# Kernel tuning notes

Measured on AMD Instinct MI355X. Metric: run time of the kernel, lower is better.

## Reference

```python
import jax, jax.numpy as jnp
import numpy as np
from jax import lax

B, C, H, W = 8, 128, 64, 64
L = H * W  # 4096, multiple of 64 so BiMamba2's pad-to-chunk is a no-op
DM, DI, DS, DC, NH, HD = 32, 64, 64, 4, 1, 64  # d_model, d_inner, d_state, d_conv, nheads, headdim


def setup_inputs() -> dict:
    key = jax.random.key(0)
    ks = jax.random.split(key, 12)
    def r(i, shape, s):
        return jax.random.normal(ks[i], shape, jnp.float32) * s
    return {
        "x": jax.random.normal(ks[0], (B, C, H, W), jnp.float32),
        "lin1_w": r(1, (C, C), 0.05), "lin1_b": jnp.zeros((C,), jnp.float32),
        "dw_w": r(2, (C, 1, 3, 3), 0.1), "dw_b": jnp.zeros((C,), jnp.float32),
        "fc_in_w": r(3, (C, DM), 0.05),
        "mam_in_w": r(4, (2, DM, 2 * DI + 2 * DS + NH), 0.05),
        "mam_conv_w": r(5, (2, DI + 2 * DS, DC), 0.1),
        "mam_conv_b": jnp.zeros((2, DI + 2 * DS), jnp.float32),
        "mam_dt_bias": r(6, (2, NH), 0.1),
        "mam_A_log": jnp.zeros((2, NH), jnp.float32),
        "mam_D": jnp.ones((2, NH), jnp.float32),
        "mam_norm_w": jnp.ones((2, DI), jnp.float32),
        "mam_out_w": r(7, (2, DI, DM), 0.05),
        "fc_out_w": r(8, (DM, C), 0.05),
        "bn_g": jnp.ones((C,), jnp.float32), "bn_b": jnp.zeros((C,), jnp.float32),
        "conv4_w": r(9, (C, C), 0.05), "conv4_b": jnp.zeros((C,), jnp.float32),
    }


def _causal_dwconv1d(x, w, b):
    # x: (B, L, Ch); w: (Ch, DC) depthwise causal kernel (torch Conv1d groups=Ch, pad=DC-1, trimmed)
    xc = jnp.transpose(x, (0, 2, 1))
    xc = jnp.pad(xc, ((0, 0), (0, 0), (DC - 1, 0)))
    o = lax.conv_general_dilated(xc, w[:, None, :], (1,), "VALID",
                                 feature_group_count=w.shape[0],
                                 dimension_numbers=("NCH", "OIH", "NCH"))
    return jnp.transpose(o + b[None, :, None], (0, 2, 1))


def _mamba2(u, W_in, conv_w, conv_b, dt_bias, A_log, D, norm_w, W_out):
    # u: (B, L, DM). Minimal Mamba2 block: in_proj -> causal dwconv/silu -> selective scan -> gated RMSNorm -> out_proj
    b, l, _ = u.shape
    zxbcdt = u @ W_in                         # (b, l, 2*DI + 2*DS + NH)
    z = zxbcdt[..., :DI]
    xBC = zxbcdt[..., DI:DI + DI + 2 * DS]
    dt = zxbcdt[..., -NH:]
    xBC = jax.nn.silu(_causal_dwconv1d(xBC, conv_w, conv_b))
    xs = xBC[..., :DI]
    Bm = xBC[..., DI:DI + DS]                 # (b, l, DS)
    Cm = xBC[..., DI + DS:]                   # (b, l, DS)
    dt = jax.nn.softplus(dt + dt_bias)        # (b, l, NH)
    dA = jnp.exp(dt * (-jnp.exp(A_log)))      # (b, l, NH)
    xh = xs.reshape(b, l, NH, HD)
    dtx = dt[..., None] * xh                  # (b, l, NH, HD)

    def step(h, inp):
        dA_t, dtx_t, B_t, C_t = inp
        h = dA_t[:, :, None, None] * h + dtx_t[..., None] * B_t[:, None, None, :]
        y = jnp.einsum("bhpn,bn->bhp", h, C_t)
        return h, y

    h0 = jnp.zeros((b, NH, HD, DS), u.dtype)
    _, ys = lax.scan(step, h0, (jnp.moveaxis(dA, 1, 0), jnp.moveaxis(dtx, 1, 0),
                                jnp.moveaxis(Bm, 1, 0), jnp.moveaxis(Cm, 1, 0)))
    y = jnp.moveaxis(ys, 0, 1) + D[None, None, :, None] * xh   # (b, l, NH, HD)
    y = y.reshape(b, l, DI)
    y = y * jax.nn.silu(z)                    # gated RMSNorm
    y = y * lax.rsqrt(jnp.mean(y * y, -1, keepdims=True) + 1e-5) * norm_w
    return y @ W_out                          # (b, l, DM)


def _forward(x, lin1_w, lin1_b, dw_w, dw_b, fc_in_w, mam_in_w, mam_conv_w, mam_conv_b,
             mam_dt_bias, mam_A_log, mam_D, mam_norm_w, mam_out_w, fc_out_w,
             bn_g, bn_b, conv4_w, conv4_b):
    b, c, h, w = x.shape
    o = jnp.einsum("bihw,io->bohw", x, lin1_w) + lin1_b[None, :, None, None]
    o = lax.conv_general_dilated(o, dw_w, (1, 1), "SAME", feature_group_count=c,
                                 dimension_numbers=("NCHW", "OIHW", "NCHW")) + dw_b[None, :, None, None]
    o = jax.nn.silu(o)
    # BiMamba2_2D: flatten HxW -> sequence, fc_in, forward + reversed Mamba2, fc_out
    s = jnp.einsum("bcl,cd->bld", o.reshape(b, c, h * w), fc_in_w)
    y1 = _mamba2(s, mam_in_w[0], mam_conv_w[0], mam_conv_b[0], mam_dt_bias[0],
                 mam_A_log[0], mam_D[0], mam_norm_w[0], mam_out_w[0])
    y2 = jnp.flip(_mamba2(jnp.flip(s, 1), mam_in_w[1], mam_conv_w[1], mam_conv_b[1],
                          mam_dt_bias[1], mam_A_log[1], mam_D[1], mam_norm_w[1], mam_out_w[1]), 1)
    o = jnp.transpose((y1 + y2) @ fc_out_w, (0, 2, 1)).reshape(b, c, h, w)
    # BatchNorm2d (training-mode batch statistics)
    mu = jnp.mean(o, (0, 2, 3), keepdims=True)
    var = jnp.mean((o - mu) ** 2, (0, 2, 3), keepdims=True)
    o = (o - mu) * lax.rsqrt(var + 1e-5) * bn_g[None, :, None, None] + bn_b[None, :, None, None]
    g = jax.nn.sigmoid(jnp.einsum("bihw,io->bohw", o, conv4_w) + conv4_b[None, :, None, None])
    return g * x + x


def reference(x, lin1_w, lin1_b, dw_w, dw_b, fc_in_w, mam_in_w, mam_conv_w, mam_conv_b,
              mam_dt_bias, mam_A_log, mam_D, mam_norm_w, mam_out_w, fc_out_w,
              bn_g, bn_b, conv4_w, conv4_b):
    return _forward(x, lin1_w, lin1_b, dw_w, dw_b, fc_in_w, mam_in_w, mam_conv_w, mam_conv_b,
                    mam_dt_bias, mam_A_log, mam_D, mam_norm_w, mam_out_w, fc_out_w,
                    bn_g, bn_b, conv4_w, conv4_b)
```

## Files before the change

kernel.cpp:

```cpp
#include <hip/hip_runtime.h>
#include <math.h>

constexpr int Bn = 8, Cn = 128, Ln = 4096;

constexpr size_t OFF_O1   = 0;
constexpr size_t OFF_O2   = 4194304;
constexpr size_t OFF_S    = 8388608;
constexpr size_t OFF_Z    = 9437184;
constexpr size_t OFF_WT   = 11534336;
constexpr size_t OFF_XBCA = 13631488;
constexpr size_t OFF_DTS  = 26214400;
constexpr size_t OFF_CUM  = 26279936;
constexpr size_t OFF_T    = 26345472;
constexpr size_t OFF_SPREV= 30539776;
constexpr size_t OFF_S2A  = 34734080;
constexpr size_t OFF_S2B  = 35782656;
constexpr size_t OFF_BN   = 36831232;
constexpr size_t OFF_O3   = 0;

constexpr long XSTRIDE_H = 6291456;
constexpr long TSTRIDE = 2097152;

typedef __attribute__((ext_vector_type(8))) short short8;
typedef __attribute__((ext_vector_type(4))) float f32x4;
typedef __attribute__((ext_vector_type(4))) unsigned short us4;
typedef __attribute__((ext_vector_type(8))) unsigned short us8;

__device__ __forceinline__ float siluf(float v) { return v / (1.0f + expf(-v)); }

__device__ __forceinline__ unsigned short tobf(float f) {
  unsigned int u = __float_as_uint(f);
  u += 0x7FFFu + ((u >> 16) & 1u);
  return (unsigned short)(u >> 16);
}

__device__ __forceinline__ float frombf(unsigned short u) {
  return __uint_as_float(((unsigned int)u) << 16);
}

__device__ __forceinline__ unsigned int pk2(float a, float b) {
  return (unsigned int)tobf(a) | ((unsigned int)tobf(b) << 16);
}

__device__ __forceinline__ short8 ldfrag(const unsigned short* p) {
  union { unsigned int u[4]; short8 s; } cv;
  cv.u[0] = *(const unsigned int*)(p);
  cv.u[1] = *(const unsigned int*)(p + 2);
  cv.u[2] = *(const unsigned int*)(p + 4);
  cv.u[3] = *(const unsigned int*)(p + 6);
  return cv.s;
}

__global__ __launch_bounds__(256) void k_lin1(const float* __restrict__ x,
                                              const float* __restrict__ w,
                                              const float* __restrict__ bias,
                                              unsigned short* __restrict__ o1) {
  __shared__ unsigned short wT[64][140];
  __shared__ unsigned short xT[64][140];
  int b = blockIdx.y, l0 = blockIdx.x * 64, cb = blockIdx.z * 64;
  int tid = threadIdx.x, lane = tid & 63, mt = tid >> 6;
  int q = lane >> 4, i = lane & 15;
  int c4 = (tid & 15) * 4, k0 = (tid >> 4) * 2;
#pragma unroll
  for (int s = 0; s < 4; ++s) {
    int k = k0 + s * 32;
    float4 w0 = *(const float4*)&w[k * 128 + cb + c4];
    float4 w1 = *(const float4*)&w[(k + 1) * 128 + cb + c4];
    *(unsigned int*)&wT[c4 + 0][k] = pk2(w0.x, w1.x);
    *(unsigned int*)&wT[c4 + 1][k] = pk2(w0.y, w1.y);
    *(unsigned int*)&wT[c4 + 2][k] = pk2(w0.z, w1.z);
    *(unsigned int*)&wT[c4 + 3][k] = pk2(w0.w, w1.w);
    float4 x0 = *(const float4*)&x[((long)b * 128 + k) * 4096 + l0 + c4];
    float4 x1 = *(const float4*)&x[((long)b * 128 + k + 1) * 4096 + l0 + c4];
    *(unsigned int*)&xT[c4 + 0][k] = pk2(x0.x, x1.x);
    *(unsigned int*)&xT[c4 + 1][k] = pk2(x0.y, x1.y);
    *(unsigned int*)&xT[c4 + 2][k] = pk2(x0.z, x1.z);
    *(unsigned int*)&xT[c4 + 3][k] = pk2(x0.w, x1.w);
  }
  __syncthreads();
  short8 af[4];
#pragma unroll
  for (int kk = 0; kk < 4; ++kk)
    af[kk] = ldfrag(&wT[mt * 16 + i][q * 8 + 32 * kk]);
  float bv[4];
#pragma unroll
  for (int r2 = 0; r2 < 4; ++r2) bv[r2] = bias[cb + 16 * mt + q * 4 + r2];
#pragma unroll
  for (int nt = 0; nt < 4; ++nt) {
    f32x4 d = {0.f, 0.f, 0.f, 0.f};
#pragma unroll
    for (int kk = 0; kk < 4; ++kk) {
      short8 bfr = ldfrag(&xT[nt * 16 + i][q * 8 + 32 * kk]);
      d = __builtin_amdgcn_mfma_f32_16x16x32_bf16(af[kk], bfr, d, 0, 0, 0);
    }
#pragma unroll
    for (int r2 = 0; r2 < 4; ++r2) {
      int c = 16 * mt + q * 4 + r2;
      o1[((long)b * 128 + cb + c) * 4096 + l0 + nt * 16 + i] = tobf(d[r2] + bv[r2]);
    }
  }
}

__global__ void k_dw(const unsigned short* __restrict__ o1,
                     const float* __restrict__ wgt,
                     const float* __restrict__ bias, unsigned short* __restrict__ o2) {
  __shared__ float p[4096];
  int bc = blockIdx.x, c = bc & 127, tid = threadIdx.x;
  const unsigned short* src = o1 + (long)bc * 4096;
#pragma unroll
  for (int s4 = 0; s4 < 2; ++s4) {
    int off = s4 * 2048 + tid * 8;
    us8 v = *(const us8*)&src[off];
#pragma unroll
    for (int j = 0; j < 8; ++j) p[off + j] = frombf(v[j]);
  }
  float wr[9];
#pragma unroll
  for (int j = 0; j < 9; ++j) wr[j] = wgt[c * 9 + j];
  float bv = bias[c];
  __syncthreads();
  int wg = tid & 15, hs = tid >> 4;
  int w0 = wg * 4, h0 = hs * 4;
  float in[6][6];
#pragma unroll
  for (int ri = 0; ri < 6; ++ri) {
    int h = h0 - 1 + ri;
    if (h < 0 || h > 63) {
#pragma unroll
      for (int ci = 0; ci < 6; ++ci) in[ri][ci] = 0.f;
    } else {
      float4 cc = *(float4*)&p[h * 64 + w0];
      in[ri][1] = cc.x; in[ri][2] = cc.y; in[ri][3] = cc.z; in[ri][4] = cc.w;
      in[ri][0] = (w0 > 0) ? p[h * 64 + w0 - 1] : 0.f;
      in[ri][5] = (w0 < 60) ? p[h * 64 + w0 + 4] : 0.f;
    }
  }
#pragma unroll
  for (int r = 0; r < 4; ++r) {
    us4 oc;
#pragma unroll
    for (int q = 0; q < 4; ++q) {
      float acc = bv;
#pragma unroll
      for (int dh = 0; dh < 3; ++dh)
#pragma unroll
        for (int dq = 0; dq < 3; ++dq)
          acc += in[r + dh][q + dq] * wr[dh * 3 + dq];
      oc[q] = tobf(siluf(acc));
    }
    *(us4*)&o2[(long)bc * 4096 + (h0 + r) * 64 + w0] = oc;
  }
}

__global__ void k_fcin(const unsigned short* __restrict__ o2, const float* __restrict__ w,
                       unsigned short* __restrict__ sb,
                       const float* __restrict__ Win, unsigned short* __restrict__ WT) {
  __shared__ float xt[128][64];
  __shared__ float wt[128][32];
  int b = blockIdx.y, l0 = blockIdx.x * 64;
  int tid = threadIdx.x;
  int f4 = (tid & 15) * 4, r0 = tid >> 4;
#pragma unroll
  for (int st = 0; st < 8; ++st) {
    int r = r0 + st * 16;
    us4 v = *(const us4*)&o2[((long)b * 128 + r) * 4096 + l0 + f4];
#pragma unroll
    for (int j = 0; j < 4; ++j) xt[r][f4 + j] = frombf(v[j]);
  }
  int f4w = (tid & 7) * 4, rw = tid >> 3;
#pragma unroll
  for (int st = 0; st < 4; ++st) {
    int r = rw + st * 32;
    *(float4*)&wt[r][f4w] = *(const float4*)&w[r * 32 + f4w];
  }
  __syncthreads();
  int tx = tid & 15, ty = tid >> 4;
  int c0 = tx * 4, d0 = ty * 2;
  float acc[2][4] = {};
  for (int k = 0; k < 128; ++k) {
    float4 xv = *(float4*)&xt[k][c0];
    float2 wv = *(float2*)&wt[k][d0];
    float xa[4] = {xv.x, xv.y, xv.z, xv.w};
#pragma unroll
    for (int q = 0; q < 4; ++q) {
      acc[0][q] += wv.x * xa[q];
      acc[1][q] += wv.y * xa[q];
    }
  }
#pragma unroll
  for (int q = 0; q < 4; ++q) {
    long ob = ((long)b * 4096 + l0 + c0 + q) * 32 + d0;
    *(unsigned int*)&sb[ob] = pk2(acc[0][q], acc[1][q]);
  }
  if (blockIdx.y == 0 && blockIdx.x < 2) {
    int dir = blockIdx.x;
    for (int idx = tid; idx < 272 * 32; idx += 256) {
      int n = idx >> 5, kk = idx & 31;
      float v = (n < 257) ? Win[dir * 32 * 257 + kk * 257 + n] : 0.f;
      WT[dir * 8704 + idx] = tobf(v);
    }
  }
}

__global__ __launch_bounds__(256) void k_inprojconv(
    const unsigned short* __restrict__ sb, const unsigned short* __restrict__ WT,
    const float* __restrict__ conv_w, const float* __restrict__ conv_b,
    const float* __restrict__ dt_bias, const float* __restrict__ A_log,
    unsigned short* __restrict__ zT, unsigned short* __restrict__ xbca,
    float* __restrict__ dts, float* __restrict__ cum, float* __restrict__ Tg) {
  __shared__ unsigned short xbcT[192][82];
  __shared__ float fXf[64][68];
  __shared__ float dtL[64];
  __shared__ float dtsS[64], cumSS[64], fL[64];
  int dir = blockIdx.z, b = blockIdx.y, l0 = blockIdx.x * 64;
  int tid = threadIdx.x, lane = tid & 63, mt = tid >> 6;
  int q = lane >> 4, i = lane & 15;
  long rowbase = (long)b * 4096 + l0;
  const unsigned short* W = WT + (long)dir * 8704;
  const short8 zfrag = {0, 0, 0, 0, 0, 0, 0, 0};

  if (mt == 0) {
    short8 afr[4];
#pragma unroll
    for (int rt = 0; rt < 4; ++rt) {
      int l = l0 + 16 * rt + i;
      int lsrc = dir ? (4095 - l) : l;
      afr[rt] = *(const short8*)&sb[((long)b * 4096 + lsrc) * 32 + q * 8];
    }
#pragma unroll
    for (int ct = 0; ct < 4; ++ct) {
      int n = 16 * ct + i;
      short8 bfr = *(const short8*)&W[n * 32 + q * 8];
      unsigned short* zrow = zT + (((long)dir * 64 + n) * 8 + b) * 4096 + l0 + q * 4;
#pragma unroll
      for (int rt = 0; rt < 4; ++rt) {
        f32x4 d = {0.f, 0.f, 0.f, 0.f};
        d = __builtin_amdgcn_mfma_f32_16x16x32_bf16(afr[rt], bfr, d, 0, 0, 0);
        us4 pk;
        pk[0] = tobf(d[0]); pk[1] = tobf(d[1]);
        pk[2] = tobf(d[2]); pk[3] = tobf(d[3]);
        *(us4*)&zrow[16 * rt] = pk;
      }
    }
    {
      short8 bfr = *(const short8*)&W[(256 + i) * 32 + q * 8];
#pragma unroll
      for (int rt = 0; rt < 4; ++rt) {
        f32x4 d = {0.f, 0.f, 0.f, 0.f};
        d = __builtin_amdgcn_mfma_f32_16x16x32_bf16(afr[rt], bfr, d, 0, 0, 0);
        if (i == 0) {
#pragma unroll
          for (int r2 = 0; r2 < 4; ++r2) dtL[16 * rt + q * 4 + r2] = d[r2];
        }
      }
    }
  } else {
    short8 afr[5];
#pragma unroll
    for (int rt = 0; rt < 5; ++rt) {
      int l = l0 - 3 + 16 * rt + i;
      if (l >= 0 && l < 4096) {
        int lsrc = dir ? (4095 - l) : l;
        afr[rt] = *(const short8*)&sb[((long)b * 4096 + lsrc) * 32 + q * 8];
      } else {
        afr[rt] = zfrag;
      }
    }
#pragma unroll
    for (int cti = 0; cti < 4; ++cti) {
      int n = 16 * (mt * 4 + cti) + i;
      short8 bfr = *(const short8*)&W[n * 32 + q * 8];
      int cc = n - 64;
#pragma unroll
      for (int rt = 0; rt < 5; ++rt) {
        f32x4 d = {0.f, 0.f, 0.f, 0.f};
        d = __builtin_amdgcn_mfma_f32_16x16x32_bf16(afr[rt], bfr, d, 0, 0, 0);
        int rr0 = 16 * rt + q * 4;
        unsigned int p0 = (unsigned int)tobf(d[0]) | ((unsigned int)tobf(d[1]) << 16);
        unsigned int p1 = (unsigned int)tobf(d[2]) | ((unsigned int)tobf(d[3]) << 16);
        *(unsigned int*)&xbcT[cc][rr0] = p0;
        *(unsigned int*)&xbcT[cc][rr0 + 2] = p1;
      }
    }
  }
  __syncthreads();

  if (tid < 192) {
    int c = tid;
    float cw0 = conv_w[dir * 768 + c * 4 + 0];
    float cw1 = conv_w[dir * 768 + c * 4 + 1];
    float cw2 = conv_w[dir * 768 + c * 4 + 2];
    float cw3 = conv_w[dir * 768 + c * 4 + 3];
    float cb2 = conv_b[dir * 192 + c];
    unsigned short* xp = xbca + (long)dir * XSTRIDE_H;
    float win0 = 0.f, win1 = 0.f, win2 = 0.f, win3 = 0.f;
    for (int rp = 0; rp < 34; ++rp) {
      unsigned int pk = *(const unsigned int*)&xbcT[c][rp * 2];
      float a0 = frombf((unsigned short)(pk & 0xFFFFu));
      float a1 = frombf((unsigned short)(pk >> 16));
      int rr = rp * 2;
      win0 = win1; win1 = win2; win2 = win3; win3 = a0;
      if (rr >= 3 && rr <= 66) {
        float acc = cb2 + win0 * cw0 + win1 * cw1 + win2 * cw2 + win3 * cw3;
        float sv = siluf(acc);
        int t = rr - 3;
        xp[(rowbase + t) * 192 + c] = tobf(sv);
        if (c < 64) fXf[c][t] = sv;
        else if (c < 128) xbcT[c][t] = tobf(sv);
      }
      win0 = win1; win1 = win2; win2 = win3; win3 = a1;
      if (rr + 1 >= 3 && rr + 1 <= 66) {
        float acc = cb2 + win0 * cw0 + win1 * cw1 + win2 * cw2 + win3 * cw3;
        float sv = siluf(acc);
        int t = rr - 2;
        xp[(rowbase + t) * 192 + c] = tobf(sv);
        if (c < 64) fXf[c][t] = sv;
        else if (c < 128) xbcT[c][t] = tobf(sv);
      }
    }
  } else {
    int ln = tid - 192;
    float v = dtL[ln] + dt_bias[dir];
    float sp = (v > 20.f) ? v : log1pf(expf(v));
    dts[dir * 32768 + rowbase + ln] = sp;
    dtsS[ln] = sp;
    float cd = -expf(A_log[dir]) * sp;
#pragma unroll
    for (int off = 1; off < 64; off <<= 1) {
      float u = __shfl_up(cd, off);
      if (ln >= off) cd += u;
    }
    cum[dir * 32768 + rowbase + ln] = cd;
    cumSS[ln] = cd;
  }
  __syncthreads();

  if (tid < 64) fL[tid] = expf(cumSS[63] - cumSS[tid]) * dtsS[tid];
  __syncthreads();

  {
    int c = tid & 63, tb2 = (tid >> 6) * 16;
#pragma unroll
    for (int j = 0; j < 8; ++j) {
      int t = tb2 + 2 * j;
      float2 v = *(const float2*)&fXf[c][t];
      unsigned int pk = (unsigned int)tobf(v.x * fL[t]) |
                        ((unsigned int)tobf(v.y * fL[t + 1]) << 16);
      *(unsigned int*)&xbcT[c][t] = pk;
    }
  }
  __syncthreads();

  {
    short8 a0 = ldfrag(&xbcT[mt * 16 + i][q * 8]);
    short8 a1 = ldfrag(&xbcT[mt * 16 + i][q * 8 + 32]);
    float* Tp = Tg + (long)dir * TSTRIDE + ((long)(b * 64 + blockIdx.x)) * 4096;
#pragma unroll
    for (int nt = 0; nt < 4; ++nt) {
      short8 b0 = ldfrag(&xbcT[64 + nt * 16 + i][q * 8]);
      short8 b1 = ldfrag(&xbcT[64 + nt * 16 + i][q * 8 + 32]);
      f32x4 d = {0.f, 0.f, 0.f, 0.f};
      d = __builtin_amdgcn_mfma_f32_16x16x32_bf16(a0, b0, d, 0, 0, 0);
      d = __builtin_amdgcn_mfma_f32_16x16x32_bf16(a1, b1, d, 0, 0, 0);
#pragma unroll
      for (int r2 = 0; r2 < 4; ++r2)
        Tp[(mt * 16 + q * 4 + r2) * 64 + nt * 16 + i] = d[r2];
    }
  }
}

__global__ void k_scan(const float* __restrict__ T, const float* __restrict__ cum,
                       unsigned short* __restrict__ Sprev) {
  __shared__ float E[64];
  int blk = blockIdx.x;
  int dirb = blk >> 3;
  int dir = dirb >> 3, b = dirb & 7;
  int pn = (blk & 7) * 512 + threadIdx.x * 2;
  const float* cp = cum + dir * 32768 + b * 4096;
  if (threadIdx.x < 64) E[threadIdx.x] = expf(cp[threadIdx.x * 64 + 63]);
  __syncthreads();
  const float* Tp = T + (long)dir * TSTRIDE + (long)b * 262144 + pn;
  unsigned short* Sp = Sprev + (long)dir * TSTRIDE + (long)b * 262144 + pn;
  float s0 = 0.f, s1 = 0.f;
  float2 tb[16];
#pragma unroll
  for (int j = 0; j < 16; ++j) tb[j] = *(const float2*)&Tp[(long)j * 4096];
  for (int kc = 0; kc < 4; ++kc) {
    float2 tn[16];
    if (kc < 3) {
#pragma unroll
      for (int j = 0; j < 16; ++j)
        tn[j] = *(const float2*)&Tp[(long)(kc * 16 + 16 + j) * 4096];
    }
#pragma unroll
    for (int j = 0; j < 16; ++j) {
      int k = kc * 16 + j;
      *(unsigned int*)&Sp[(long)k * 4096] = pk2(s0, s1);
      s0 = fmaf(E[k], s0, tb[j].x);
      s1 = fmaf(E[k], s1, tb[j].y);
    }
    if (kc < 3) {
#pragma unroll
      for (int j = 0; j < 16; ++j) tb[j] = tn[j];
    }
  }
}

__global__ __launch_bounds__(256) void k_chunkYout(
    const unsigned short* __restrict__ xbca, const float* __restrict__ dts,
    const float* __restrict__ cum, const unsigned short* __restrict__ Sprev,
    const float* __restrict__ Dp, const unsigned short* __restrict__ zT,
    const float* __restrict__ normw, const float* __restrict__ Wout,
    float* __restrict__ s2a, float* __restrict__ s2b) {
  __shared__ unsigned short Cb[64][72];
  __shared__ unsigned short Bop[64][68];
  __shared__ unsigned short Gb[64][72];
  __shared__ unsigned short WnT[32][66];
  __shared__ float cumS[64];
  int dir = blockIdx.y;
  int bk = blockIdx.x, b = bk >> 6, k = bk & 63;
  int tid = threadIdx.x, lane = tid & 63, mt = tid >> 6;
  int q = lane >> 4, i = lane & 15;
  const unsigned short* xp = xbca + (long)dir * XSTRIDE_H;
  const float* dtp = dts + dir * 32768;
  const float* cp = cum + dir * 32768;
  const unsigned short* Sp = Sprev + (long)dir * TSTRIDE;
  long base = (long)b * 4096 + (long)k * 64;

  {
    int c4 = (tid & 15) * 4, r0 = tid >> 4;
#pragma unroll
    for (int s = 0; s < 4; ++s) {
      int r = r0 + s * 16;
      float dtv = dtp[base + r];
      const unsigned short* rowp = &xp[(base + r) * 192 + 64];
      us4 bv = *(const us4*)&rowp[c4];
      us4 cv = *(const us4*)&rowp[64 + c4];
      us4 bo;
#pragma unroll
      for (int j = 0; j < 4; ++j) bo[j] = tobf(frombf(bv[j]) * dtv);
      *(us4*)&Bop[r][c4] = bo;
      *(us4*)&Cb[r][c4] = cv;
    }
  }
  for (int idx = tid; idx < 2048; idx += 256) {
    int p = idx >> 5, d = idx & 31;
    WnT[d][p] = tobf(normw[dir * 64 + p] * Wout[(long)dir * 2048 + p * 32 + d]);
  }
  if (tid < 64) cumS[tid] = cp[base + tid];
  __syncthreads();

  short8 a0 = *(const short8*)&Cb[mt * 16 + i][q * 8];
  short8 a1 = *(const short8*)&Cb[mt * 16 + i][q * 8 + 32];

#pragma unroll
  for (int lt = 0; lt < 4; ++lt) {
    short8 b0 = ldfrag(&Bop[lt * 16 + i][q * 8]);
    short8 b1 = ldfrag(&Bop[lt * 16 + i][q * 8 + 32]);
    f32x4 d = {0.f, 0.f, 0.f, 0.f};
    d = __builtin_amdgcn_mfma_f32_16x16x32_bf16(a0, b0, d, 0, 0, 0);
    d = __builtin_amdgcn_mfma_f32_16x16x32_bf16(a1, b1, d, 0, 0, 0);
#pragma unroll
    for (int r2 = 0; r2 < 4; ++r2) {
      int t = mt * 16 + q * 4 + r2;
      int l = lt * 16 + i;
      float g = (l <= t) ? d[r2] * expf(cumS[t] - cumS[l]) : 0.f;
      Gb[t][l] = tobf(g);
    }
  }
  __syncthreads();

  {
    int c4 = (tid & 15) * 4, r0 = tid >> 4;
#pragma unroll
    for (int s = 0; s < 4; ++s) {
      int r = r0 + s * 16;
      us4 sv = *(const us4*)&Sp[(long)bk * 4096 + r * 64 + c4];
      *(us4*)&Bop[r][c4] = sv;
    }
  }
  __syncthreads();

  f32x4 dint[4];
#pragma unroll
  for (int lt = 0; lt < 4; ++lt) {
    short8 b0 = ldfrag(&Bop[lt * 16 + i][q * 8]);
    short8 b1 = ldfrag(&Bop[lt * 16 + i][q * 8 + 32]);
    f32x4 d = {0.f, 0.f, 0.f, 0.f};
    d = __builtin_amdgcn_mfma_f32_16x16x32_bf16(a0, b0, d, 0, 0, 0);
    d = __builtin_amdgcn_mfma_f32_16x16x32_bf16(a1, b1, d, 0, 0, 0);
    dint[lt] = d;
  }
  __syncthreads();

#pragma unroll
  for (int j = 0; j < 8; ++j) {
    int s = mt * 16 + 2 * j;
    unsigned int pk = (unsigned int)xp[(base + s) * 192 + lane] |
                      ((unsigned int)xp[(base + s + 1) * 192 + lane] << 16);
    *(unsigned int*)&Bop[lane][s] = pk;
  }
  __syncthreads();

  short8 g0 = *(const short8*)&Gb[mt * 16 + i][q * 8];
  short8 g1 = *(const short8*)&Gb[mt * 16 + i][q * 8 + 32];
  float Dv = Dp[dir];
  float et4[4];
#pragma unroll
  for (int r2 = 0; r2 < 4; ++r2) et4[r2] = expf(cumS[mt * 16 + q * 4 + r2]);
  float yv[4][4];
  float rowss[4] = {0.f, 0.f, 0.f, 0.f};
#pragma unroll
  for (int lt = 0; lt < 4; ++lt) {
    short8 b0 = ldfrag(&Bop[lt * 16 + i][q * 8]);
    short8 b1 = ldfrag(&Bop[lt * 16 + i][q * 8 + 32]);
    f32x4 d = {0.f, 0.f, 0.f, 0.f};
    d = __builtin_amdgcn_mfma_f32_16x16x32_bf16(g0, b0, d, 0, 0, 0);
    d = __builtin_amdgcn_mfma_f32_16x16x32_bf16(g1, b1, d, 0, 0, 0);
    us4 zq = *(const us4*)&zT[(((long)dir * 64 + lt * 16 + i) * 8 + b) * 4096 +
                              (long)k * 64 + mt * 16 + q * 4];
    unsigned int xpk0 = *(const unsigned int*)&Bop[lt * 16 + i][mt * 16 + q * 4];
    unsigned int xpk1 = *(const unsigned int*)&Bop[lt * 16 + i][mt * 16 + q * 4 + 2];
    float xvr[4];
    xvr[0] = frombf((unsigned short)(xpk0 & 0xFFFFu));
    xvr[1] = frombf((unsigned short)(xpk0 >> 16));
    xvr[2] = frombf((unsigned short)(xpk1 & 0xFFFFu));
    xvr[3] = frombf((unsigned short)(xpk1 >> 16));
#pragma unroll
    for (int r2 = 0; r2 < 4; ++r2) {
      float y = d[r2] + et4[r2] * dint[lt][r2] + Dv * xvr[r2];
      float zv = frombf(zq[r2]);
      float v = y * siluf(zv);
      yv[lt][r2] = v;
      rowss[r2] += v * v;
    }
  }
#pragma unroll
  for (int m = 1; m < 16; m <<= 1) {
#pragma unroll
    for (int r2 = 0; r2 < 4; ++r2) rowss[r2] += __shfl_xor(rowss[r2], m);
  }
  float rscv[4];
#pragma unroll
  for (int r2 = 0; r2 < 4; ++r2)
    rscv[r2] = rsqrtf(rowss[r2] * (1.0f / 64.0f) + 1e-5f);
#pragma unroll
  for (int lt = 0; lt < 4; ++lt)
#pragma unroll
    for (int r2 = 0; r2 < 4; ++r2) {
      int t = mt * 16 + q * 4 + r2;
      int p = lt * 16 + i;
      Gb[t][p] = tobf(yv[lt][r2] * rscv[r2]);
    }
  __syncthreads();

  short8 y0 = *(const short8*)&Gb[mt * 16 + i][q * 8];
  short8 y1 = *(const short8*)&Gb[mt * 16 + i][q * 8 + 32];
  float* s2x = dir ? s2b : s2a;
#pragma unroll
  for (int dt = 0; dt < 2; ++dt) {
    short8 b0 = ldfrag(&WnT[dt * 16 + i][q * 8]);
    short8 b1 = ldfrag(&WnT[dt * 16 + i][q * 8 + 32]);
    f32x4 d = {0.f, 0.f, 0.f, 0.f};
    d = __builtin_amdgcn_mfma_f32_16x16x32_bf16(y0, b0, d, 0, 0, 0);
    d = __builtin_amdgcn_mfma_f32_16x16x32_bf16(y1, b1, d, 0, 0, 0);
#pragma unroll
    for (int r2 = 0; r2 < 4; ++r2) {
      int tl = mt * 16 + q * 4 + r2;
      int l = k * 64 + tl;
      int lout = dir ? (4095 - l) : l;
      int dd = dt * 16 + i;
      s2x[((long)b * 4096 + lout) * 32 + dd] = d[r2];
    }
  }
}

__global__ void k_fcout(const float* __restrict__ s2a, const float* __restrict__ s2b,
                        const float* __restrict__ w, unsigned short* __restrict__ o3,
                        float* __restrict__ part) {
  __shared__ float st[32][68];
  __shared__ float wt[32][64];
  int b = blockIdx.y, l0 = blockIdx.x * 64, cb = blockIdx.z * 64;
  int tid = threadIdx.x;
  {
    int d = tid & 31, l = tid >> 5;
    for (int si = 0; si < 8; ++si) {
      int ll = l + si * 8;
      long o = ((long)b * 4096 + l0 + ll) * 32 + d;
      st[d][ll] = s2a[o] + s2b[o];
    }
    int f4 = (tid & 15) * 4, r = tid >> 4;
    for (int si = 0; si < 2; ++si) {
      int rr = r + si * 16;
      *(float4*)&wt[rr][f4] = *(const float4*)&w[rr * 128 + cb + f4];
    }
  }
  __syncthreads();
  int tx = tid & 15, ty = tid >> 4;
  int c0 = tx * 4, t0 = ty * 4;
  float acc[4][4] = {};
  for (int k = 0; k < 32; ++k) {
    float4 xv = *(float4*)&st[k][c0];
    float4 wv = *(float4*)&wt[k][t0];
    float xa[4] = {xv.x, xv.y, xv.z, xv.w};
    float wa[4] = {wv.x, wv.y, wv.z, wv.w};
#pragma unroll
    for (int a = 0; a < 4; ++a)
#pragma unroll
      for (int q = 0; q < 4; ++q) acc[a][q] += wa[a] * xa[q];
  }
#pragma unroll
  for (int a = 0; a < 4; ++a) {
    us4 pk;
#pragma unroll
    for (int q = 0; q < 4; ++q) pk[q] = tobf(acc[a][q]);
    *(us4*)&o3[((long)b * 128 + cb + t0 + a) * 4096 + l0 + c0] = pk;
  }
  float ssum[4], sqq[4];
#pragma unroll
  for (int a = 0; a < 4; ++a) {
    ssum[a] = acc[a][0] + acc[a][1] + acc[a][2] + acc[a][3];
    sqq[a] = acc[a][0] * acc[a][0] + acc[a][1] * acc[a][1] +
             acc[a][2] * acc[a][2] + acc[a][3] * acc[a][3];
  }
#pragma unroll
  for (int m = 1; m < 16; m <<= 1) {
#pragma unroll
    for (int a = 0; a < 4; ++a) {
      ssum[a] += __shfl_xor(ssum[a], m);
      sqq[a] += __shfl_xor(sqq[a], m);
    }
  }
  if (tx == 0) {
    int idx = b * 64 + blockIdx.x;
#pragma unroll
    for (int a = 0; a < 4; ++a) {
      int ch = cb + t0 + a;
      part[(long)ch * 512 + idx] = ssum[a];
      part[65536 + (long)ch * 512 + idx] = sqq[a];
    }
  }
}

__global__ void k_bnred(const float* __restrict__ part, float* __restrict__ stats) {
  int ch = blockIdx.x, tid = threadIdx.x;
  float s = part[(long)ch * 512 + tid] + part[(long)ch * 512 + 256 + tid];
  float q = part[65536 + (long)ch * 512 + tid] +
            part[65536 + (long)ch * 512 + 256 + tid];
  for (int off = 32; off; off >>= 1) {
    s += __shfl_down(s, off);
    q += __shfl_down(q, off);
  }
  __shared__ float rs[4], rq[4];
  if ((tid & 63) == 0) { rs[tid >> 6] = s; rq[tid >> 6] = q; }
  __syncthreads();
  if (tid == 0) {
    stats[ch] = rs[0] + rs[1] + rs[2] + rs[3];
    stats[128 + ch] = rq[0] + rq[1] + rq[2] + rq[3];
  }
}

__global__ __launch_bounds__(256) void k_final(const unsigned short* __restrict__ o3,
                                               const float* __restrict__ stats,
                                               const float* __restrict__ bng,
                                               const float* __restrict__ bnb,
                                               const float* __restrict__ w,
                                               const float* __restrict__ bias,
                                               const float* __restrict__ x,
                                               float* __restrict__ out) {
  __shared__ unsigned short wT[64][140];
  __shared__ unsigned short aT[64][140];
  __shared__ float sc[128], sh[128];
  int b = blockIdx.y, l0 = blockIdx.x * 64, cb = blockIdx.z * 64;
  int tid = threadIdx.x, lane = tid & 63, mt = tid >> 6;
  int q = lane >> 4, i = lane & 15;
  if (tid < 128) {
    float mu = stats[tid] * (1.0f / 32768.0f);
    float var = stats[128 + tid] * (1.0f / 32768.0f) - mu * mu;
    float r = rsqrtf(var + 1e-5f);
    sc[tid] = r * bng[tid];
    sh[tid] = bnb[tid] - mu * r * bng[tid];
  }
  __syncthreads();
  int c4 = (tid & 15) * 4, k0 = (tid >> 4) * 2;
#pragma unroll
  for (int s = 0; s < 4; ++s) {
    int k = k0 + s * 32;
    float4 w0 = *(const float4*)&w[k * 128 + cb + c4];
    float4 w1 = *(const float4*)&w[(k + 1) * 128 + cb + c4];
    *(unsigned int*)&wT[c4 + 0][k] = pk2(w0.x, w1.x);
    *(unsigned int*)&wT[c4 + 1][k] = pk2(w0.y, w1.y);
    *(unsigned int*)&wT[c4 + 2][k] = pk2(w0.z, w1.z);
    *(unsigned int*)&wT[c4 + 3][k] = pk2(w0.w, w1.w);
    us4 a0 = *(const us4*)&o3[((long)b * 128 + k) * 4096 + l0 + c4];
    us4 a1 = *(const us4*)&o3[((long)b * 128 + k + 1) * 4096 + l0 + c4];
    float sc0 = sc[k], sh0 = sh[k], sc1 = sc[k + 1], sh1 = sh[k + 1];
#pragma unroll
    for (int j = 0; j < 4; ++j) {
      *(unsigned int*)&aT[c4 + j][k] =
          pk2(fmaf(frombf(a0[j]), sc0, sh0), fmaf(frombf(a1[j]), sc1, sh1));
    }
  }
  __syncthreads();
  short8 af[4];
#pragma unroll
  for (int kk = 0; kk < 4; ++kk)
    af[kk] = ldfrag(&wT[mt * 16 + i][q * 8 + 32 * kk]);
  float bv[4];
#pragma unroll
  for (int r2 = 0; r2 < 4; ++r2) bv[r2] = bias[cb + 16 * mt + q * 4 + r2];
#pragma unroll
  for (int nt = 0; nt < 4; ++nt) {
    f32x4 d = {0.f, 0.f, 0.f, 0.f};
#pragma unroll
    for (int kk = 0; kk < 4; ++kk) {
      short8 bfr = ldfrag(&aT[nt * 16 + i][q * 8 + 32 * kk]);
      d = __builtin_amdgcn_mfma_f32_16x16x32_bf16(af[kk], bfr, d, 0, 0, 0);
    }
#pragma unroll
    for (int r2 = 0; r2 < 4; ++r2) {
      int c = 16 * mt + q * 4 + r2;
      long xi = ((long)b * 128 + cb + c) * 4096 + l0 + nt * 16 + i;
      float g = 1.0f / (1.0f + expf(-(d[r2] + bv[r2])));
      out[xi] = x[xi] * (1.0f + g);
    }
  }
}

extern "C" void kernel_launch(void* const* d_in, const int* in_sizes, int n_in,
                              void* d_out, int out_size, void* d_ws, size_t ws_size,
                              hipStream_t stream) {
  const float* x          = (const float*)d_in[0];
  const float* lin1_w     = (const float*)d_in[1];
  const float* lin1_b     = (const float*)d_in[2];
  const float* dw_w       = (const float*)d_in[3];
  const float* dw_b       = (const float*)d_in[4];
  const float* fc_in_w    = (const float*)d_in[5];
  const float* mam_in_w   = (const float*)d_in[6];
  const float* mam_conv_w = (const float*)d_in[7];
  const float* mam_conv_b = (const float*)d_in[8];
  const float* mam_dt_bias= (const float*)d_in[9];
  const float* mam_A_log  = (const float*)d_in[10];
  const float* mam_D      = (const float*)d_in[11];
  const float* mam_norm_w = (const float*)d_in[12];
  const float* mam_out_w  = (const float*)d_in[13];
  const float* fc_out_w   = (const float*)d_in[14];
  const float* bn_g       = (const float*)d_in[15];
  const float* bn_b       = (const float*)d_in[16];
  const float* conv4_w    = (const float*)d_in[17];
  const float* conv4_b    = (const float*)d_in[18];
  float* out = (float*)d_out;
  float* ws  = (float*)d_ws;

  unsigned short* o1h  = (unsigned short*)(ws + OFF_O1);
  unsigned short* o2h  = (unsigned short*)(ws + OFF_O2);
  unsigned short* sbuf = (unsigned short*)(ws + OFF_S);
  unsigned short* zTb  = (unsigned short*)(ws + OFF_Z);
  unsigned short* WTb  = (unsigned short*)(ws + OFF_WT);
  unsigned short* xbca = (unsigned short*)(ws + OFF_XBCA);
  float* dts  = ws + OFF_DTS;
  float* cum  = ws + OFF_CUM;
  float* Tbuf = ws + OFF_T;
  unsigned short* Sprev = (unsigned short*)(ws + OFF_SPREV);
  float* s2a  = ws + OFF_S2A;
  float* s2b  = ws + OFF_S2B;
  float* bnst = ws + OFF_BN;
  unsigned short* o3h = (unsigned short*)(ws + OFF_O3);
  float* part = ws + OFF_T;

  k_lin1<<<dim3(64, 8, 2), 256, 0, stream>>>(x, lin1_w, lin1_b, o1h);
  k_dw<<<1024, 256, 0, stream>>>(o1h, dw_w, dw_b, o2h);
  k_fcin<<<dim3(64, 8), 256, 0, stream>>>(o2h, fc_in_w, sbuf, mam_in_w, WTb);
  k_inprojconv<<<dim3(64, 8, 2), 256, 0, stream>>>(sbuf, WTb, mam_conv_w, mam_conv_b,
                                                   mam_dt_bias, mam_A_log,
                                                   zTb, xbca, dts, cum, Tbuf);
  k_scan<<<128, 256, 0, stream>>>(Tbuf, cum, Sprev);
  k_chunkYout<<<dim3(512, 2), 256, 0, stream>>>(xbca, dts, cum, Sprev, mam_D, zTb,
                                                mam_norm_w, mam_out_w, s2a, s2b);
  k_fcout<<<dim3(64, 8, 2), 256, 0, stream>>>(s2a, s2b, fc_out_w, o3h, part);
  k_bnred<<<128, 256, 0, stream>>>(part, bnst);
  k_final<<<dim3(64, 8, 2), 256, 0, stream>>>(o3h, bnst, bn_g, bn_b, conv4_w, conv4_b, x, out);
}
```

Baseline: 201.4 us.

## Store chunk states and mamba outputs in bf16, restructure scan and chunkYout LDS

```diff
diff --git a/kernel.cpp b/kernel.cpp
--- a/kernel.cpp
+++ b/kernel.cpp
@@ -207,7 +207,8 @@
     const float* __restrict__ conv_w, const float* __restrict__ conv_b,
     const float* __restrict__ dt_bias, const float* __restrict__ A_log,
     unsigned short* __restrict__ zT, unsigned short* __restrict__ xbca,
-    float* __restrict__ dts, float* __restrict__ cum, float* __restrict__ Tg) {
+    float* __restrict__ dts, float* __restrict__ cum,
+    unsigned short* __restrict__ Tg) {
   __shared__ unsigned short xbcT[192][82];
   __shared__ float fXf[64][68];
   __shared__ float dtL[64];
@@ -354,7 +355,7 @@
   {
     short8 a0 = ldfrag(&xbcT[mt * 16 + i][q * 8]);
     short8 a1 = ldfrag(&xbcT[mt * 16 + i][q * 8 + 32]);
-    float* Tp = Tg + (long)dir * TSTRIDE + ((long)(b * 64 + blockIdx.x)) * 4096;
+    unsigned short* Tp = Tg + (long)dir * TSTRIDE + ((long)(b * 64 + blockIdx.x)) * 4096;
 #pragma unroll
     for (int nt = 0; nt < 4; ++nt) {
       short8 b0 = ldfrag(&xbcT[64 + nt * 16 + i][q * 8]);
@@ -364,40 +365,39 @@
       d = __builtin_amdgcn_mfma_f32_16x16x32_bf16(a1, b1, d, 0, 0, 0);
 #pragma unroll
       for (int r2 = 0; r2 < 4; ++r2)
-        Tp[(mt * 16 + q * 4 + r2) * 64 + nt * 16 + i] = d[r2];
-    }
-  }
-}
-
-__global__ void k_scan(const float* __restrict__ T, const float* __restrict__ cum,
+        Tp[(mt * 16 + q * 4 + r2) * 64 + nt * 16 + i] = tobf(d[r2]);
+    }
+  }
+}
+
+__global__ void k_scan(const unsigned short* __restrict__ T, const float* __restrict__ cum,
                        unsigned short* __restrict__ Sprev) {
   __shared__ float E[64];
   int blk = blockIdx.x;
-  int dirb = blk >> 3;
+  int dirb = blk >> 4;
   int dir = dirb >> 3, b = dirb & 7;
-  int pn = (blk & 7) * 512 + threadIdx.x * 2;
+  int pn = (blk & 15) * 256 + threadIdx.x;
   const float* cp = cum + dir * 32768 + b * 4096;
   if (threadIdx.x < 64) E[threadIdx.x] = expf(cp[threadIdx.x * 64 + 63]);
   __syncthreads();
-  const float* Tp = T + (long)dir * TSTRIDE + (long)b * 262144 + pn;
+  const unsigned short* Tp = T + (long)dir * TSTRIDE + (long)b * 262144 + pn;
   unsigned short* Sp = Sprev + (long)dir * TSTRIDE + (long)b * 262144 + pn;
-  float s0 = 0.f, s1 = 0.f;
-  float2 tb[16];
-#pragma unroll
-  for (int j = 0; j < 16; ++j) tb[j] = *(const float2*)&Tp[(long)j * 4096];
+  float s0 = 0.f;
+  float tb[16];
+#pragma unroll
+  for (int j = 0; j < 16; ++j) tb[j] = frombf(Tp[(long)j * 4096]);
   for (int kc = 0; kc < 4; ++kc) {
-    float2 tn[16];
+    float tn[16];
     if (kc < 3) {
 #pragma unroll
       for (int j = 0; j < 16; ++j)
-        tn[j] = *(const float2*)&Tp[(long)(kc * 16 + 16 + j) * 4096];
+        tn[j] = frombf(Tp[(long)(kc * 16 + 16 + j) * 4096]);
     }
 #pragma unroll
     for (int j = 0; j < 16; ++j) {
       int k = kc * 16 + j;
-      *(unsigned int*)&Sp[(long)k * 4096] = pk2(s0, s1);
-      s0 = fmaf(E[k], s0, tb[j].x);
-      s1 = fmaf(E[k], s1, tb[j].y);
+      Sp[(long)k * 4096] = tobf(s0);
+      s0 = fmaf(E[k], s0, tb[j]);
     }
     if (kc < 3) {
 #pragma unroll
@@ -411,9 +411,11 @@
     const float* __restrict__ cum, const unsigned short* __restrict__ Sprev,
     const float* __restrict__ Dp, const unsigned short* __restrict__ zT,
     const float* __restrict__ normw, const float* __restrict__ Wout,
-    float* __restrict__ s2a, float* __restrict__ s2b) {
+    unsigned short* __restrict__ s2a, unsigned short* __restrict__ s2b) {
   __shared__ unsigned short Cb[64][72];
-  __shared__ unsigned short Bop[64][68];
+  __shared__ unsigned short Bb[64][68];
+  __shared__ unsigned short Sv[64][68];
+  __shared__ unsigned short Xt[64][68];
   __shared__ unsigned short Gb[64][72];
   __shared__ unsigned short WnT[32][66];
   __shared__ float cumS[64];
@@ -436,12 +438,21 @@
       const unsigned short* rowp = &xp[(base + r) * 192 + 64];
       us4 bv = *(const us4*)&rowp[c4];
       us4 cv = *(const us4*)&rowp[64 + c4];
+      us4 sv = *(const us4*)&Sp[(long)bk * 4096 + r * 64 + c4];
       us4 bo;
 #pragma unroll
       for (int j = 0; j < 4; ++j) bo[j] = tobf(frombf(bv[j]) * dtv);
-      *(us4*)&Bop[r][c4] = bo;
+      *(us4*)&Bb[r][c4] = bo;
       *(us4*)&Cb[r][c4] = cv;
-    }
+      *(us4*)&Sv[r][c4] = sv;
+    }
+  }
+#pragma unroll
+  for (int j = 0; j < 8; ++j) {
+    int s = mt * 16 + 2 * j;
+    unsigned int pk = (unsigned int)xp[(base + s) * 192 + lane] |
+                      ((unsigned int)xp[(base + s + 1) * 192 + lane] << 16);
+    *(unsigned int*)&Xt[lane][s] = pk;
   }
   for (int idx = tid; idx < 2048; idx += 256) {
     int p = idx >> 5, d = idx & 31;
@@ -453,10 +464,21 @@
   short8 a0 = *(const short8*)&Cb[mt * 16 + i][q * 8];
   short8 a1 = *(const short8*)&Cb[mt * 16 + i][q * 8 + 32];
 
+  f32x4 dint[4];
 #pragma unroll
   for (int lt = 0; lt < 4; ++lt) {
-    short8 b0 = ldfrag(&Bop[lt * 16 + i][q * 8]);
-    short8 b1 = ldfrag(&Bop[lt * 16 + i][q * 8 + 32]);
+    short8 b0 = ldfrag(&Sv[lt * 16 + i][q * 8]);
+    short8 b1 = ldfrag(&Sv[lt * 16 + i][q * 8 + 32]);
+    f32x4 d = {0.f, 0.f, 0.f, 0.f};
+    d = __builtin_amdgcn_mfma_f32_16x16x32_bf16(a0, b0, d, 0, 0, 0);
+    d = __builtin_amdgcn_mfma_f32_16x16x32_bf16(a1, b1, d, 0, 0, 0);
+    dint[lt] = d;
+  }
+
+#pragma unroll
+  for (int lt = 0; lt < 4; ++lt) {
+    short8 b0 = ldfrag(&Bb[lt * 16 + i][q * 8]);
+    short8 b1 = ldfrag(&Bb[lt * 16 + i][q * 8 + 32]);
     f32x4 d = {0.f, 0.f, 0.f, 0.f};
     d = __builtin_amdgcn_mfma_f32_16x16x32_bf16(a0, b0, d, 0, 0, 0);
     d = __builtin_amdgcn_mfma_f32_16x16x32_bf16(a1, b1, d, 0, 0, 0);
@@ -468,39 +490,6 @@
       Gb[t][l] = tobf(g);
     }
   }
-  __syncthreads();
-
-  {
-    int c4 = (tid & 15) * 4, r0 = tid >> 4;
-#pragma unroll
-    for (int s = 0; s < 4; ++s) {
-      int r = r0 + s * 16;
-      us4 sv = *(const us4*)&Sp[(long)bk * 4096 + r * 64 + c4];
-      *(us4*)&Bop[r][c4] = sv;
-    }
-  }
-  __syncthreads();
-
-  f32x4 dint[4];
-#pragma unroll
-  for (int lt = 0; lt < 4; ++lt) {
-    short8 b0 = ldfrag(&Bop[lt * 16 + i][q * 8]);
-    short8 b1 = ldfrag(&Bop[lt * 16 + i][q * 8 + 32]);
-    f32x4 d = {0.f, 0.f, 0.f, 0.f};
-    d = __builtin_amdgcn_mfma_f32_16x16x32_bf16(a0, b0, d, 0, 0, 0);
-    d = __builtin_amdgcn_mfma_f32_16x16x32_bf16(a1, b1, d, 0, 0, 0);
-    dint[lt] = d;
-  }
-  __syncthreads();
-
-#pragma unroll
-  for (int j = 0; j < 8; ++j) {
-    int s = mt * 16 + 2 * j;
-    unsigned int pk = (unsigned int)xp[(base + s) * 192 + lane] |
-                      ((unsigned int)xp[(base + s + 1) * 192 + lane] << 16);
-    *(unsigned int*)&Bop[lane][s] = pk;
-  }
-  __syncthreads();
 
   short8 g0 = *(const short8*)&Gb[mt * 16 + i][q * 8];
   short8 g1 = *(const short8*)&Gb[mt * 16 + i][q * 8 + 32];
@@ -512,15 +501,15 @@
   float rowss[4] = {0.f, 0.f, 0.f, 0.f};
 #pragma unroll
   for (int lt = 0; lt < 4; ++lt) {
-    short8 b0 = ldfrag(&Bop[lt * 16 + i][q * 8]);
-    short8 b1 = ldfrag(&Bop[lt * 16 + i][q * 8 + 32]);
+    short8 b0 = ldfrag(&Xt[lt * 16 + i][q * 8]);
+    short8 b1 = ldfrag(&Xt[lt * 16 + i][q * 8 + 32]);
     f32x4 d = {0.f, 0.f, 0.f, 0.f};
     d = __builtin_amdgcn_mfma_f32_16x16x32_bf16(g0, b0, d, 0, 0, 0);
     d = __builtin_amdgcn_mfma_f32_16x16x32_bf16(g1, b1, d, 0, 0, 0);
     us4 zq = *(const us4*)&zT[(((long)dir * 64 + lt * 16 + i) * 8 + b) * 4096 +
                               (long)k * 64 + mt * 16 + q * 4];
-    unsigned int xpk0 = *(const unsigned int*)&Bop[lt * 16 + i][mt * 16 + q * 4];
-    unsigned int xpk1 = *(const unsigned int*)&Bop[lt * 16 + i][mt * 16 + q * 4 + 2];
+    unsigned int xpk0 = *(const unsigned int*)&Xt[lt * 16 + i][mt * 16 + q * 4];
+    unsigned int xpk1 = *(const unsigned int*)&Xt[lt * 16 + i][mt * 16 + q * 4 + 2];
     float xvr[4];
     xvr[0] = frombf((unsigned short)(xpk0 & 0xFFFFu));
     xvr[1] = frombf((unsigned short)(xpk0 >> 16));
@@ -552,11 +541,10 @@
       int p = lt * 16 + i;
       Gb[t][p] = tobf(yv[lt][r2] * rscv[r2]);
     }
-  __syncthreads();
 
   short8 y0 = *(const short8*)&Gb[mt * 16 + i][q * 8];
   short8 y1 = *(const short8*)&Gb[mt * 16 + i][q * 8 + 32];
-  float* s2x = dir ? s2b : s2a;
+  unsigned short* s2x = dir ? s2b : s2a;
 #pragma unroll
   for (int dt = 0; dt < 2; ++dt) {
     short8 b0 = ldfrag(&WnT[dt * 16 + i][q * 8]);
@@ -570,12 +558,13 @@
       int l = k * 64 + tl;
       int lout = dir ? (4095 - l) : l;
       int dd = dt * 16 + i;
-      s2x[((long)b * 4096 + lout) * 32 + dd] = d[r2];
-    }
-  }
-}
-
-__global__ void k_fcout(const float* __restrict__ s2a, const float* __restrict__ s2b,
+      s2x[((long)b * 4096 + lout) * 32 + dd] = tobf(d[r2]);
+    }
+  }
+}
+
+__global__ void k_fcout(const unsigned short* __restrict__ s2a,
+                        const unsigned short* __restrict__ s2b,
                         const float* __restrict__ w, unsigned short* __restrict__ o3,
                         float* __restrict__ part) {
   __shared__ float st[32][68];
@@ -587,7 +576,7 @@
     for (int si = 0; si < 8; ++si) {
       int ll = l + si * 8;
       long o = ((long)b * 4096 + l0 + ll) * 32 + d;
-      st[d][ll] = s2a[o] + s2b[o];
+      st[d][ll] = frombf(s2a[o]) + frombf(s2b[o]);
     }
     int f4 = (tid & 15) * 4, r = tid >> 4;
     for (int si = 0; si < 2; ++si) {
@@ -760,10 +749,10 @@
   unsigned short* xbca = (unsigned short*)(ws + OFF_XBCA);
   float* dts  = ws + OFF_DTS;
   float* cum  = ws + OFF_CUM;
-  float* Tbuf = ws + OFF_T;
+  unsigned short* Tbufh = (unsigned short*)(ws + OFF_T);
   unsigned short* Sprev = (unsigned short*)(ws + OFF_SPREV);
-  float* s2a  = ws + OFF_S2A;
-  float* s2b  = ws + OFF_S2B;
+  unsigned short* s2a = (unsigned short*)(ws + OFF_S2A);
+  unsigned short* s2b = (unsigned short*)(ws + OFF_S2B);
   float* bnst = ws + OFF_BN;
   unsigned short* o3h = (unsigned short*)(ws + OFF_O3);
   float* part = ws + OFF_T;
@@ -773,8 +762,8 @@
   k_fcin<<<dim3(64, 8), 256, 0, stream>>>(o2h, fc_in_w, sbuf, mam_in_w, WTb);
   k_inprojconv<<<dim3(64, 8, 2), 256, 0, stream>>>(sbuf, WTb, mam_conv_w, mam_conv_b,
                                                    mam_dt_bias, mam_A_log,
-                                                   zTb, xbca, dts, cum, Tbuf);
-  k_scan<<<128, 256, 0, stream>>>(Tbuf, cum, Sprev);
+                                                   zTb, xbca, dts, cum, Tbufh);
+  k_scan<<<256, 256, 0, stream>>>(Tbufh, cum, Sprev);
   k_chunkYout<<<dim3(512, 2), 256, 0, stream>>>(xbca, dts, cum, Sprev, mam_D, zTb,
                                                 mam_norm_w, mam_out_w, s2a, s2b);
   k_fcout<<<dim3(64, 8, 2), 256, 0, stream>>>(s2a, s2b, fc_out_w, o3h, part);
```

After: 206.4 us. 1.02x slower.
